# Optimization experiments

Measured on AMD Instinct MI355X. Metric: run time of the kernel, lower is better.

The kernel has to match this reference:

```python
import jax, jax.numpy as jnp
import numpy as np

B, S, D, H = 2, 2048, 1024, 16
DK = D // H


def setup_inputs() -> dict:
    key = jax.random.key(0)
    ks = jax.random.split(key, 12)
    scale = 0.02
    inp = {
        "query": jax.random.normal(ks[0], (B, S, D), jnp.float32),
        "key": jax.random.normal(ks[1], (B, S, D), jnp.float32),
        "value": jax.random.normal(ks[2], (B, S, D), jnp.float32),
        "mask": jax.random.randint(ks[3], (B, S), 0, 2, jnp.int32),
        "Wq": jax.random.normal(ks[4], (D, D), jnp.float32) * scale,
        "bq": jnp.zeros((D,), jnp.float32),
        "Wk": jax.random.normal(ks[5], (D, D), jnp.float32) * scale,
        "bk": jnp.zeros((D,), jnp.float32),
        "Wv": jax.random.normal(ks[6], (D, D), jnp.float32) * scale,
        "bv": jnp.zeros((D,), jnp.float32),
        "Wo": jax.random.normal(ks[7], (D, D), jnp.float32) * scale,
        "bo": jnp.zeros((D,), jnp.float32),
    }
    return inp


def reference(query, key, value, mask, Wq, bq, Wk, bk, Wv, bv, Wo, bo):
    # Linear projections then split heads: [B, S, D] -> [B, H, S, DK]
    def proj(x, W, b):
        y = x @ W.T + b  # torch nn.Linear: x @ W^T + b
        return y.reshape(B, S, H, DK).transpose(0, 2, 1, 3)

    q = proj(query, Wq, bq)
    k = proj(key, Wk, bk)
    v = proj(value, Wv, bv)

    # Scaled dot-product attention with full [B, H, S, S] scores (naive form)
    scores = jnp.einsum("bhqd,bhkd->bhqk", q, k) / jnp.sqrt(jnp.float32(DK))
    # mask==1 marks padding over key positions; broadcast [B,1,1,S]
    pad = (mask == 1)[:, None, None, :]
    scores = jnp.where(pad, -jnp.inf, scores)
    p_attn = jax.nn.softmax(scores, axis=-1)
    # dropout omitted (eval / deterministic mode)
    x = jnp.einsum("bhqk,bhkd->bhqd", p_attn, v)
    x = x.transpose(0, 2, 1, 3).reshape(B, S, D)
    return x @ Wo.T + bo
```

## Files before the change

### kernel.cpp

```cpp
#include <hip/hip_runtime.h>
#include <stdint.h>

typedef short bf16x8 __attribute__((ext_vector_type(8)));
typedef float f32x4  __attribute__((ext_vector_type(4)));
typedef unsigned int u32x2 __attribute__((ext_vector_type(2)));
typedef unsigned short u16;

#define BB 2
#define SS 2048
#define DD 1024
#define HH 16
#define NTOK (BB*SS)
#define QSC 0.18033688f

__device__ __forceinline__ u16 f2bf(float f) {
  union { float f; uint32_t u; } c; c.f = f;
  uint32_t r = c.u + 0x7FFFu + ((c.u >> 16) & 1u);
  return (u16)(r >> 16);
}

__device__ __forceinline__ void gll16(const void* g, void* l) {
  __builtin_amdgcn_global_load_lds((__attribute__((address_space(1))) void*)(void*)g,
                                   (__attribute__((address_space(3))) void*)l, 16, 0, 0);
}

struct CvtArgs { const float* src[4]; u16* dst[4]; int n; };
__global__ void cvtn_kernel(CvtArgs a) {
  const float* __restrict__ src = a.src[blockIdx.z];
  u16* __restrict__ dst = a.dst[blockIdx.z];
  int i = (blockIdx.x * blockDim.x + threadIdx.x) * 4;
  const int stride = gridDim.x * blockDim.x * 4;
  for (; i < a.n; i += stride) {
    float4 v = *(const float4*)(src + i);
    ushort4 o;
    o.x = f2bf(v.x); o.y = f2bf(v.y); o.z = f2bf(v.z); o.w = f2bf(v.w);
    *(ushort4*)(dst + i) = o;
  }
}

__global__ __launch_bounds__(256) void maskcnt_kernel(const int* __restrict__ mask,
                                                      float* __restrict__ out) {
  const int b = blockIdx.x, t = threadIdx.x;
  const int4 v1 = *(const int4*)(mask + b * SS + t * 8);
  const int4 v2 = *(const int4*)(mask + b * SS + t * 8 + 4);
  int s = v1.x + v1.y + v1.z + v1.w + v2.x + v2.y + v2.z + v2.w;
#pragma unroll
  for (int off = 32; off; off >>= 1) s += __shfl_xor(s, off);
  __shared__ int red[4];
  if ((t & 63) == 0) red[t >> 6] = s;
  __syncthreads();
  if (t == 0) out[b] = (float)(red[0] + red[1] + red[2] + red[3]);
}

template<int MODE>
__device__ __forceinline__ void gemm_bt_body(const u16* __restrict__ A,
                                             const u16* __restrict__ W,
                                             const float* __restrict__ bias,
                                             const int* __restrict__ mask,
                                             void* __restrict__ Cout,
                                             u16* As, u16* Bs) {
  const int tid = threadIdx.x;
  const int lane = tid & 63, wid = tid >> 6;
  const int r16 = lane & 15, g4 = lane >> 4;
  const int m0 = blockIdx.y * 128, n0 = blockIdx.x * 128;
  const int wm = (wid >> 1) * 64, wn = (wid & 1) * 64;

  const f32x4 zero = {0.f, 0.f, 0.f, 0.f};
  f32x4 acc[4][4];
#pragma unroll
  for (int i = 0; i < 4; ++i)
#pragma unroll
    for (int j = 0; j < 4; ++j) acc[i][j] = zero;

  const int row0 = tid >> 2, blk0 = tid & 3;
  auto stage = [&](int kt, int buf) {
#pragma unroll
    for (int it = 0; it < 2; ++it) {
      const int row = row0 + it * 64;
      const int sb = blk0 ^ (row & 3);
      gll16(A + (size_t)(m0 + row) * DD + kt * 32 + sb * 8,
            As + buf * 4096 + (tid + it * 256) * 8);
      gll16(W + (size_t)(n0 + row) * DD + kt * 32 + sb * 8,
            Bs + buf * 4096 + (tid + it * 256) * 8);
    }
  };

  stage(0, 0);
  __syncthreads();

  for (int kt = 0; kt < DD / 32; ++kt) {
    const int cur = kt & 1;
    if (kt + 1 < DD / 32) stage(kt + 1, cur ^ 1);

    bf16x8 af[4], bfr[4];
#pragma unroll
    for (int i = 0; i < 4; ++i) {
      const int ar = wm + i * 16 + r16;
      af[i] = *(const bf16x8*)(As + cur * 4096 + ar * 32 + ((g4 ^ (ar & 3)) << 3));
      const int br = wn + i * 16 + r16;
      bfr[i] = *(const bf16x8*)(Bs + cur * 4096 + br * 32 + ((g4 ^ (br & 3)) << 3));
    }
#pragma unroll
    for (int i = 0; i < 4; ++i)
#pragma unroll
      for (int j = 0; j < 4; ++j)
        acc[i][j] = __builtin_amdgcn_mfma_f32_16x16x32_bf16(af[i], bfr[j], acc[i][j], 0, 0, 0);
    __syncthreads();
  }

  float bcol[4];
#pragma unroll
  for (int j = 0; j < 4; ++j) bcol[j] = bias[n0 + wn + j * 16 + r16];

#pragma unroll
  for (int i = 0; i < 4; ++i) {
    const int rowb = m0 + wm + i * 16 + g4 * 4;
    int mr[4] = {0, 0, 0, 0};
    if (MODE == 1 || MODE == 2) {
      const int4 mv = *(const int4*)(mask + rowb);
      mr[0] = mv.x; mr[1] = mv.y; mr[2] = mv.z; mr[3] = mv.w;
    }
#pragma unroll
    for (int j = 0; j < 4; ++j) {
      const int col = n0 + wn + j * 16 + r16;
      if (MODE == 3) {
#pragma unroll
        for (int r = 0; r < 4; ++r)
          ((float*)Cout)[(size_t)(rowb + r) * DD + col] = acc[i][j][r] + bcol[j];
      } else if (MODE == 0) {
#pragma unroll
        for (int r = 0; r < 4; ++r)
          ((u16*)Cout)[(size_t)(rowb + r) * DD + col] = f2bf((acc[i][j][r] + bcol[j]) * QSC);
      } else if (MODE == 1) {
#pragma unroll
        for (int r = 0; r < 4; ++r) {
          const float v = mr[r] ? 0.f : (acc[i][j][r] + bcol[j]);
          ((u16*)Cout)[(size_t)(rowb + r) * DD + col] = f2bf(v);
        }
      } else {
        const int bb = rowb >> 11, s0 = rowb & (SS - 1);
        ushort4 pk;
        pk.x = f2bf(mr[0] ? 0.f : (acc[i][j][0] + bcol[j]));
        pk.y = f2bf(mr[1] ? 0.f : (acc[i][j][1] + bcol[j]));
        pk.z = f2bf(mr[2] ? 0.f : (acc[i][j][2] + bcol[j]));
        pk.w = f2bf(mr[3] ? 0.f : (acc[i][j][3] + bcol[j]));
        *(ushort4*)((u16*)Cout + (size_t)(bb * DD + col) * SS + s0) = pk;
      }
    }
  }
}

struct QkvArgs {
  const u16* A[3];
  const u16* W[3];
  const float* bias[3];
  const int* mask;
  u16* outq; u16* outk; u16* outv;
};

__global__ __launch_bounds__(256) void gemm_qkv_kernel(QkvArgs a) {
  __shared__ __align__(16) u16 As[2][128 * 32];
  __shared__ __align__(16) u16 Bs[2][128 * 32];
  const int z = blockIdx.z;
  if (z == 0)      gemm_bt_body<0>(a.A[0], a.W[0], a.bias[0], nullptr, (void*)a.outq, &As[0][0], &Bs[0][0]);
  else if (z == 1) gemm_bt_body<1>(a.A[1], a.W[1], a.bias[1], a.mask, (void*)a.outk, &As[0][0], &Bs[0][0]);
  else             gemm_bt_body<2>(a.A[2], a.W[2], a.bias[2], a.mask, (void*)a.outv, &As[0][0], &Bs[0][0]);
}

__global__ __launch_bounds__(256) void gemm_out_kernel(const u16* __restrict__ A,
                                                       const u16* __restrict__ W,
                                                       const float* __restrict__ bias,
                                                       float* __restrict__ C) {
  __shared__ __align__(16) u16 As[2][128 * 32];
  __shared__ __align__(16) u16 Bs[2][128 * 32];
  gemm_bt_body<3>(A, W, bias, nullptr, (void*)C, &As[0][0], &Bs[0][0]);
}

__global__ __launch_bounds__(256) void attn_kernel(const u16* __restrict__ Qp,
                                                   const u16* __restrict__ Kp,
                                                   const u16* __restrict__ Vt,
                                                   const float* __restrict__ padcnt,
                                                   u16* __restrict__ ctx) {
  __shared__ __align__(16) u16 Ks[2][64 * 64];
  __shared__ __align__(16) u16 Vs[2][64 * 64];

  const int tid = threadIdx.x;
  const int lane = tid & 63, wid = tid >> 6;
  const int r16 = lane & 15, g4 = lane >> 4;
  const int qt = blockIdx.x, h = blockIdx.y, b = blockIdx.z;

  const int qtok = b * SS + qt * 64 + wid * 16 + r16;
  bf16x8 qf[2];
#pragma unroll
  for (int c = 0; c < 2; ++c)
    qf[c] = *(const bf16x8*)(Qp + (size_t)qtok * DD + h * 64 + c * 32 + g4 * 8);

  const f32x4 zero = {0.f, 0.f, 0.f, 0.f};
  f32x4 o[4];
#pragma unroll
  for (int j = 0; j < 4; ++j) o[j] = zero;
  float ll = 0.f;

  const int srow0 = tid >> 3, sblk0 = tid & 7;
  const u16* Kbase = Kp + (size_t)(b * SS) * DD + h * 64;
  const u16* Vbase = Vt + (size_t)(b * DD + h * 64) * SS;

  auto stage = [&](int kt, int buf) {
#pragma unroll
    for (int it = 0; it < 2; ++it) {
      const int row = srow0 + it * 32;
      const int sb = sblk0 ^ (row & 7);
      gll16(Kbase + (size_t)(kt * 64 + row) * DD + sb * 8, &Ks[buf][(tid + it * 256) * 8]);
      gll16(Vbase + (size_t)row * SS + kt * 64 + sb * 8, &Vs[buf][(tid + it * 256) * 8]);
    }
  };

  stage(0, 0);
  __syncthreads();

  for (int kt = 0; kt < SS / 64; ++kt) {
    const int cur = kt & 1;
    if (kt + 1 < SS / 64) stage(kt + 1, cur ^ 1);

    f32x4 st[4];
#pragma unroll
    for (int j = 0; j < 4; ++j) st[j] = zero;
#pragma unroll
    for (int c = 0; c < 2; ++c)
#pragma unroll
      for (int j = 0; j < 4; ++j) {
        const int kr = j * 16 + r16;
        const bf16x8 kf = *(const bf16x8*)(&Ks[cur][kr * 64 + (((c * 4 + g4) ^ (kr & 7)) << 3)]);
        st[j] = __builtin_amdgcn_mfma_f32_16x16x32_bf16(kf, qf[c], st[j], 0, 0, 0);
      }

    uint32_t q0[4], q1[4];
#pragma unroll
    for (int j = 0; j < 4; ++j) {
      float p0, p1, p2, p3;
      asm("v_exp_f32 %0, %1" : "=v"(p0) : "v"(st[j][0]));
      asm("v_exp_f32 %0, %1" : "=v"(p1) : "v"(st[j][1]));
      asm("v_exp_f32 %0, %1" : "=v"(p2) : "v"(st[j][2]));
      asm("v_exp_f32 %0, %1" : "=v"(p3) : "v"(st[j][3]));
      ll += (p0 + p1) + (p2 + p3);
      asm("v_cvt_pk_bf16_f32 %0, %1, %2" : "=v"(q0[j]) : "v"(p0), "v"(p1));
      asm("v_cvt_pk_bf16_f32 %0, %1, %2" : "=v"(q1[j]) : "v"(p2), "v"(p3));
    }

    bf16x8 pa[2];
#pragma unroll
    for (int c = 0; c < 2; ++c) {
      u32x2 s0 = __builtin_amdgcn_permlane32_swap(q0[2 * c], q0[2 * c + 1], false, false);
      u32x2 s1 = __builtin_amdgcn_permlane16_swap(s0.x, s0.y, false, false);
      u32x2 t0 = __builtin_amdgcn_permlane32_swap(q1[2 * c], q1[2 * c + 1], false, false);
      u32x2 t1 = __builtin_amdgcn_permlane16_swap(t0.x, t0.y, false, false);
      union { uint32_t u[4]; bf16x8 v; } cv;
      cv.u[0] = s1.x; cv.u[1] = t1.x; cv.u[2] = s1.y; cv.u[3] = t1.y;
      pa[c] = cv.v;
    }

#pragma unroll
    for (int c = 0; c < 2; ++c)
#pragma unroll
      for (int j = 0; j < 4; ++j) {
        const int vr = j * 16 + r16;
        const bf16x8 vf = *(const bf16x8*)(&Vs[cur][vr * 64 + (((c * 4 + g4) ^ (vr & 7)) << 3)]);
        o[j] = __builtin_amdgcn_mfma_f32_16x16x32_bf16(pa[c], vf, o[j], 0, 0, 0);
      }
    __syncthreads();
  }

  ll += __shfl_xor(ll, 16);
  ll += __shfl_xor(ll, 32);
  ll -= padcnt[b];
  const float inv = 1.0f / ll;
  float invr[4];
#pragma unroll
  for (int r = 0; r < 4; ++r) invr[r] = __shfl(inv, g4 * 4 + r);

  const int otok = b * SS + qt * 64 + wid * 16 + g4 * 4;
#pragma unroll
  for (int j = 0; j < 4; ++j) {
    const int col = h * 64 + j * 16 + r16;
#pragma unroll
    for (int r = 0; r < 4; ++r)
      ctx[(size_t)(otok + r) * DD + col] = f2bf(o[j][r] * invr[r]);
  }
}

extern "C" void kernel_launch(void* const* d_in, const int* in_sizes, int n_in,
                              void* d_out, int out_size, void* d_ws, size_t ws_size,
                              hipStream_t stream) {
  (void)in_sizes; (void)n_in; (void)out_size; (void)ws_size;
  const float* f_q = (const float*)d_in[0];
  const float* f_k = (const float*)d_in[1];
  const float* f_v = (const float*)d_in[2];
  const int* mask  = (const int*)d_in[3];
  const float* Wq = (const float*)d_in[4];
  const float* bq = (const float*)d_in[5];
  const float* Wk = (const float*)d_in[6];
  const float* bk = (const float*)d_in[7];
  const float* Wv = (const float*)d_in[8];
  const float* bv = (const float*)d_in[9];
  const float* Wo = (const float*)d_in[10];
  const float* bo = (const float*)d_in[11];

  char* ws = (char*)d_ws;
  const size_t XB = (size_t)NTOK * DD * 2;
  const size_t WB = (size_t)DD * DD * 2;
  u16* Xq  = (u16*)(ws);
  u16* Xk  = (u16*)(ws + XB);
  u16* Xv  = (u16*)(ws + 2 * XB);
  u16* Qp  = (u16*)(ws + 3 * XB);
  u16* Kp  = (u16*)(ws + 4 * XB);
  u16* Vt  = (u16*)(ws + 5 * XB);
  u16* Wqb = (u16*)(ws + 6 * XB);
  u16* Wkb = (u16*)(ws + 6 * XB + WB);
  u16* Wvb = (u16*)(ws + 6 * XB + 2 * WB);
  u16* Wob = (u16*)(ws + 6 * XB + 3 * WB);
  float* padcnt = (float*)(ws + 6 * XB + 4 * WB);
  u16* ctx = Xq;

  CvtArgs cx;
  cx.src[0] = f_q; cx.src[1] = f_k; cx.src[2] = f_v; cx.src[3] = f_q;
  cx.dst[0] = Xq;  cx.dst[1] = Xk;  cx.dst[2] = Xv;  cx.dst[3] = Xq;
  cx.n = NTOK * DD;
  cvtn_kernel<<<dim3(1024, 1, 3), 256, 0, stream>>>(cx);

  CvtArgs cw;
  cw.src[0] = Wq;  cw.src[1] = Wk;  cw.src[2] = Wv;  cw.src[3] = Wo;
  cw.dst[0] = Wqb; cw.dst[1] = Wkb; cw.dst[2] = Wvb; cw.dst[3] = Wob;
  cw.n = DD * DD;
  cvtn_kernel<<<dim3(256, 1, 4), 256, 0, stream>>>(cw);

  maskcnt_kernel<<<BB, 256, 0, stream>>>(mask, padcnt);

  QkvArgs qa;
  qa.A[0] = Xq;  qa.A[1] = Xk;  qa.A[2] = Xv;
  qa.W[0] = Wqb; qa.W[1] = Wkb; qa.W[2] = Wvb;
  qa.bias[0] = bq; qa.bias[1] = bk; qa.bias[2] = bv;
  qa.mask = mask;
  qa.outq = Qp; qa.outk = Kp; qa.outv = Vt;
  gemm_qkv_kernel<<<dim3(DD / 128, NTOK / 128, 3), 256, 0, stream>>>(qa);

  attn_kernel<<<dim3(SS / 64, HH, BB), 256, 0, stream>>>(Qp, Kp, Vt, padcnt, ctx);
  gemm_out_kernel<<<dim3(DD / 128, NTOK / 128), 256, 0, stream>>>(ctx, Wob, bo, (float*)d_out);
}
```

Before: 151.8 us.

## Add block swizzling, MFMA priority hints, and unroll attention loop by buffer

Block indices in the QKV GEMM, output GEMM and attention kernels are remapped so consecutive workgroups are spread across groups of eight, aiming at better L2/MALL locality or XCD distribution. MFMA sections are wrapped in s_setprio(1)/s_setprio(0) so waves issuing matrix math get scheduling priority over waves issuing loads. The attention loop is unrolled by two with compile-time buffer indices, and the first QK MFMA starts from a zero accumulator. Together these target scheduling and cache behaviour rather than arithmetic, at the cost of more complex index math and larger code size.

```diff
diff --git a/kernel.cpp b/kernel.cpp
--- a/kernel.cpp
+++ b/kernel.cpp
@@ -1,5 +1,6 @@
 #include <hip/hip_runtime.h>
 #include <stdint.h>
+#include <type_traits>
 
 typedef short bf16x8 __attribute__((ext_vector_type(8)));
 typedef float f32x4  __attribute__((ext_vector_type(4)));
@@ -58,11 +59,11 @@
                                              const float* __restrict__ bias,
                                              const int* __restrict__ mask,
                                              void* __restrict__ Cout,
+                                             int m0, int n0,
                                              u16* As, u16* Bs) {
   const int tid = threadIdx.x;
   const int lane = tid & 63, wid = tid >> 6;
   const int r16 = lane & 15, g4 = lane >> 4;
-  const int m0 = blockIdx.y * 128, n0 = blockIdx.x * 128;
   const int wm = (wid >> 1) * 64, wn = (wid & 1) * 64;
 
   const f32x4 zero = {0.f, 0.f, 0.f, 0.f};
@@ -100,11 +101,13 @@
       const int br = wn + i * 16 + r16;
       bfr[i] = *(const bf16x8*)(Bs + cur * 4096 + br * 32 + ((g4 ^ (br & 3)) << 3));
     }
+    __builtin_amdgcn_s_setprio(1);
 #pragma unroll
     for (int i = 0; i < 4; ++i)
 #pragma unroll
       for (int j = 0; j < 4; ++j)
         acc[i][j] = __builtin_amdgcn_mfma_f32_16x16x32_bf16(af[i], bfr[j], acc[i][j], 0, 0, 0);
+    __builtin_amdgcn_s_setprio(0);
     __syncthreads();
   }
 
@@ -161,10 +164,14 @@
 __global__ __launch_bounds__(256) void gemm_qkv_kernel(QkvArgs a) {
   __shared__ __align__(16) u16 As[2][128 * 32];
   __shared__ __align__(16) u16 Bs[2][128 * 32];
-  const int z = blockIdx.z;
-  if (z == 0)      gemm_bt_body<0>(a.A[0], a.W[0], a.bias[0], nullptr, (void*)a.outq, &As[0][0], &Bs[0][0]);
-  else if (z == 1) gemm_bt_body<1>(a.A[1], a.W[1], a.bias[1], a.mask, (void*)a.outk, &As[0][0], &Bs[0][0]);
-  else             gemm_bt_body<2>(a.A[2], a.W[2], a.bias[2], a.mask, (void*)a.outv, &As[0][0], &Bs[0][0]);
+  const int fid = blockIdx.x + (blockIdx.y << 3) + (blockIdx.z << 8);
+  const int swz = (fid & 7) * 96 + (fid >> 3);
+  const int z = swz >> 8;
+  const int rem = swz & 255;
+  const int m0 = (rem >> 3) * 128, n0 = (rem & 7) * 128;
+  if (z == 0)      gemm_bt_body<0>(a.A[0], a.W[0], a.bias[0], nullptr, (void*)a.outq, m0, n0, &As[0][0], &Bs[0][0]);
+  else if (z == 1) gemm_bt_body<1>(a.A[1], a.W[1], a.bias[1], a.mask, (void*)a.outk, m0, n0, &As[0][0], &Bs[0][0]);
+  else             gemm_bt_body<2>(a.A[2], a.W[2], a.bias[2], a.mask, (void*)a.outv, m0, n0, &As[0][0], &Bs[0][0]);
 }
 
 __global__ __launch_bounds__(256) void gemm_out_kernel(const u16* __restrict__ A,
@@ -173,9 +180,13 @@
                                                        float* __restrict__ C) {
   __shared__ __align__(16) u16 As[2][128 * 32];
   __shared__ __align__(16) u16 Bs[2][128 * 32];
-  gemm_bt_body<3>(A, W, bias, nullptr, (void*)C, &As[0][0], &Bs[0][0]);
-}
-
+  const int fid = blockIdx.x + (blockIdx.y << 3);
+  const int swz = (fid & 7) * 32 + (fid >> 3);
+  const int m0 = (swz >> 3) * 128, n0 = (swz & 7) * 128;
+  gemm_bt_body<3>(A, W, bias, nullptr, (void*)C, m0, n0, &As[0][0], &Bs[0][0]);
+}
+
+#define NT (SS / 64)
 __global__ __launch_bounds__(256) void attn_kernel(const u16* __restrict__ Qp,
                                                    const u16* __restrict__ Kp,
                                                    const u16* __restrict__ Vt,
@@ -187,7 +198,10 @@
   const int tid = threadIdx.x;
   const int lane = tid & 63, wid = tid >> 6;
   const int r16 = lane & 15, g4 = lane >> 4;
-  const int qt = blockIdx.x, h = blockIdx.y, b = blockIdx.z;
+  const int fid = blockIdx.x + 32 * (blockIdx.y + 16 * blockIdx.z);
+  const int swz = (fid & 7) * 128 + (fid >> 3);
+  const int qt = swz & 31, rem = swz >> 5;
+  const int h = rem & 15, b = rem >> 4;
 
   const int qtok = b * SS + qt * 64 + wid * 16 + r16;
   bf16x8 qf[2];
@@ -218,21 +232,25 @@
   stage(0, 0);
   __syncthreads();
 
-  for (int kt = 0; kt < SS / 64; ++kt) {
-    const int cur = kt & 1;
-    if (kt + 1 < SS / 64) stage(kt + 1, cur ^ 1);
+  auto tile_step = [&](auto CURC, int kt) {
+    constexpr int cur = decltype(CURC)::value;
+    if (kt + 1 < NT) stage(kt + 1, cur ^ 1);
 
     f32x4 st[4];
-#pragma unroll
-    for (int j = 0; j < 4; ++j) st[j] = zero;
-#pragma unroll
-    for (int c = 0; c < 2; ++c)
-#pragma unroll
-      for (int j = 0; j < 4; ++j) {
-        const int kr = j * 16 + r16;
-        const bf16x8 kf = *(const bf16x8*)(&Ks[cur][kr * 64 + (((c * 4 + g4) ^ (kr & 7)) << 3)]);
-        st[j] = __builtin_amdgcn_mfma_f32_16x16x32_bf16(kf, qf[c], st[j], 0, 0, 0);
-      }
+    __builtin_amdgcn_s_setprio(1);
+#pragma unroll
+    for (int j = 0; j < 4; ++j) {
+      const int kr = j * 16 + r16;
+      const bf16x8 kf = *(const bf16x8*)(&Ks[cur][kr * 64 + ((g4 ^ (kr & 7)) << 3)]);
+      st[j] = __builtin_amdgcn_mfma_f32_16x16x32_bf16(kf, qf[0], zero, 0, 0, 0);
+    }
+#pragma unroll
+    for (int j = 0; j < 4; ++j) {
+      const int kr = j * 16 + r16;
+      const bf16x8 kf = *(const bf16x8*)(&Ks[cur][kr * 64 + (((4 + g4) ^ (kr & 7)) << 3)]);
+      st[j] = __builtin_amdgcn_mfma_f32_16x16x32_bf16(kf, qf[1], st[j], 0, 0, 0);
+    }
+    __builtin_amdgcn_s_setprio(0);
 
     uint32_t q0[4], q1[4];
 #pragma unroll
@@ -259,6 +277,7 @@
       pa[c] = cv.v;
     }
 
+    __builtin_amdgcn_s_setprio(1);
 #pragma unroll
     for (int c = 0; c < 2; ++c)
 #pragma unroll
@@ -267,7 +286,13 @@
         const bf16x8 vf = *(const bf16x8*)(&Vs[cur][vr * 64 + (((c * 4 + g4) ^ (vr & 7)) << 3)]);
         o[j] = __builtin_amdgcn_mfma_f32_16x16x32_bf16(pa[c], vf, o[j], 0, 0, 0);
       }
+    __builtin_amdgcn_s_setprio(0);
     __syncthreads();
+  };
+
+  for (int kt = 0; kt < NT; kt += 2) {
+    tile_step(std::integral_constant<int, 0>{}, kt);
+    tile_step(std::integral_constant<int, 1>{}, kt + 1);
   }
 
   ll += __shfl_xor(ll, 16);
```

New measurement: 155.5 us. 1.02x slower.
